# Kernel optimization log

Measured on AMD Instinct MI355X. Metric: run time of the kernel, lower is better.

## Reference

```python
import jax, jax.numpy as jnp
import numpy as np

B, L, D = 1, 512, 1024
NH, NKV, NR = 16, 4, 16
HD, RD = 64, 64
NREP = NH // NKV  # 4
ATTN_SCALE = 1.0 / float(np.sqrt(HD))
REL_SCALE = 1.0 / float(np.sqrt(RD))


def setup_inputs() -> dict:
    key = jax.random.key(0)
    ks = jax.random.split(key, 9)
    x = jax.random.normal(ks[0], (B, L, D), jnp.float32)
    symbols = jax.random.normal(ks[1], (B, L, D), jnp.float32)
    # standard llama-style RoPE frequencies: [L, HD//2]
    inv_freq = 1.0 / (10000.0 ** (np.arange(0, HD, 2, dtype=np.float32) / HD))
    f = np.outer(np.arange(L, dtype=np.float32), inv_freq)
    freqs_cos = jnp.asarray(np.cos(f), jnp.float32)
    freqs_sin = jnp.asarray(np.sin(f), jnp.float32)
    s = 0.02
    wq_attn = jax.random.normal(ks[2], (D, NH * HD), jnp.float32) * s
    wk_attn = jax.random.normal(ks[3], (D, NKV * HD), jnp.float32) * s
    wq_rel = jax.random.normal(ks[4], (D, NR * RD), jnp.float32) * s
    wk_rel = jax.random.normal(ks[5], (D, NR * RD), jnp.float32) * s
    wr = jax.random.normal(ks[6], (NR, NH * HD), jnp.float32) * s
    wv = jax.random.normal(ks[7], (D, NKV * HD), jnp.float32) * s
    wo = jax.random.normal(ks[8], (NH * HD, NH * HD), jnp.float32) * s
    return dict(x=x, symbols=symbols, freqs_cos=freqs_cos, freqs_sin=freqs_sin,
                wq_attn=wq_attn, wk_attn=wk_attn, wq_rel=wq_rel, wk_rel=wk_rel,
                wr=wr, wv=wv, wo=wo)


def _rope(t, cos, sin):
    # t: [b, l, h, hd]; cos/sin: [l, hd//2]
    tr = t.reshape(t.shape[:-1] + (HD // 2, 2))
    re, im = tr[..., 0], tr[..., 1]
    c = cos[None, :, None, :]
    s = sin[None, :, None, :]
    out = jnp.stack([re * c - im * s, re * s + im * c], axis=-1)
    return out.reshape(t.shape)


def reference(x, symbols, freqs_cos, freqs_sin, wq_attn, wk_attn, wq_rel, wk_rel, wr, wv, wo):
    b, l, _ = x.shape
    q = (x @ wq_attn).reshape(b, l, NH, HD)
    k = (x @ wk_attn).reshape(b, l, NKV, HD)
    qr = (x @ wq_rel).reshape(b, l, NR, RD)
    kr = (x @ wk_rel).reshape(b, l, NR, RD)
    sv = (symbols @ wv).reshape(b, l, NKV, HD)
    q = _rope(q, freqs_cos, freqs_sin)
    k = _rope(k, freqs_cos, freqs_sin)
    # GQA: repeat kv heads consecutively (matches torch repeat_kv expand+reshape)
    k = jnp.repeat(k, NREP, axis=2)
    sv = jnp.repeat(sv, NREP, axis=2)
    scores = jnp.einsum('bihd,bjhd->bhij', q, k) * ATTN_SCALE
    causal = jnp.tril(jnp.ones((l, l), bool))
    scores = jnp.where(causal[None, None], scores, -jnp.inf)
    attn = jax.nn.softmax(scores, axis=-1)  # [b, nh, l, l]
    # relation scores, identity activation, laid out as [b, i, j, nr]
    relations = jnp.einsum('bird,bjrd->bijr', qr, kr) * REL_SCALE
    proj_rel = (relations @ wr).reshape(b, l, l, NH, HD)  # dominant intermediate
    attended_symbols = jnp.einsum('bhij,bjhd->bihd', attn, sv)
    attended_relations = jnp.einsum('bhij,bijhd->bihd', attn, proj_rel)
    out = (attended_symbols + attended_relations).reshape(b, l, NH * HD) @ wo
    return out, attn, relations
```

## Files before the change

kernel.cpp:

```cpp
#include <hip/hip_runtime.h>
#include <math.h>

#define ATTN_SCALE 0.125f
#define REL_SCALE 0.125f

using ushort = unsigned short;
using bf16x8 = __attribute__((ext_vector_type(8))) __bf16;
using floatx4 = __attribute__((ext_vector_type(4))) float;
using ushort8 = __attribute__((ext_vector_type(8))) ushort;
using ushort4v = __attribute__((ext_vector_type(4))) ushort;

__device__ __forceinline__ ushort f2bf(float x) {
  unsigned int u = __builtin_bit_cast(unsigned int, x);
  u += 0x7fffu + ((u >> 16) & 1u);
  return (ushort)(u >> 16);
}

__global__ __launch_bounds__(256) void prep_kernel(
    const float* __restrict__ x, const float* __restrict__ sym,
    const float* __restrict__ wq, const float* __restrict__ wk,
    const float* __restrict__ wqr, const float* __restrict__ wkr,
    const float* __restrict__ wv, const float* __restrict__ wo,
    ushort* __restrict__ xb, ushort* __restrict__ symb,
    ushort* __restrict__ wqT, ushort* __restrict__ wkT, ushort* __restrict__ wqrT,
    ushort* __restrict__ wkrT, ushort* __restrict__ wvT, ushort* __restrict__ woT) {
  if (blockIdx.z == 6) {
    int b = blockIdx.y * 32 + blockIdx.x;
    if (b >= 512) return;
    int idx = b * 256 + threadIdx.x;
    int i4 = idx << 2;
    float4 v = *(const float4*)(x + i4);
    uint2 o;
    o.x = (unsigned)f2bf(v.x) | ((unsigned)f2bf(v.y) << 16);
    o.y = (unsigned)f2bf(v.z) | ((unsigned)f2bf(v.w) << 16);
    *(uint2*)(xb + i4) = o;
    float4 w = *(const float4*)(sym + i4);
    o.x = (unsigned)f2bf(w.x) | ((unsigned)f2bf(w.y) << 16);
    o.y = (unsigned)f2bf(w.z) | ((unsigned)f2bf(w.w) << 16);
    *(uint2*)(symb + i4) = o;
    return;
  }
  __shared__ ushort t[32][33];
  const float* in;
  ushort* out;
  int N;
  switch (blockIdx.z) {
    case 0: in = wq;  out = wqT;  N = 1024; break;
    case 1: in = wk;  out = wkT;  N = 256;  break;
    case 2: in = wqr; out = wqrT; N = 1024; break;
    case 3: in = wkr; out = wkrT; N = 1024; break;
    case 4: in = wv;  out = wvT;  N = 256;  break;
    default: in = wo; out = woT;  N = 1024; break;
  }
  int n0 = blockIdx.x << 5;
  if (n0 >= N) return;
  int k0 = blockIdx.y << 5;
  int tx = threadIdx.x & 31, ty = threadIdx.x >> 5;
#pragma unroll
  for (int rr = 0; rr < 32; rr += 8)
    t[ty + rr][tx] = f2bf(in[(size_t)(k0 + ty + rr) * N + n0 + tx]);
  __syncthreads();
#pragma unroll
  for (int rr = 0; rr < 32; rr += 8)
    out[(size_t)(n0 + ty + rr) * 1024 + k0 + tx] = t[tx][ty + rr];
}

__global__ __launch_bounds__(256) void proj_mfma(
    const ushort* __restrict__ xb, const ushort* __restrict__ symb,
    const ushort* __restrict__ wqT, const ushort* __restrict__ wkT,
    const ushort* __restrict__ wqrT, const ushort* __restrict__ wkrT,
    const ushort* __restrict__ wvT,
    ushort* __restrict__ qb, ushort* __restrict__ kb, ushort* __restrict__ qrb,
    ushort* __restrict__ krb, ushort* __restrict__ svT,
    const float* __restrict__ fcos, const float* __restrict__ fsin) {
  __shared__ ushort As[64][72];
  __shared__ ushort Bs[32][72];
  const int z = blockIdx.z;
  const ushort* A = xb;
  const ushort* Bt;
  ushort* C;
  int N;
  switch (z) {
    case 0: Bt = wqT;  C = qb;  N = 1024; break;
    case 1: Bt = wkT;  C = kb;  N = 256;  break;
    case 2: Bt = wqrT; C = qrb; N = 1024; break;
    case 3: Bt = wkrT; C = krb; N = 1024; break;
    default: A = symb; Bt = wvT; C = svT; N = 256; break;
  }
  const int bn = blockIdx.x << 5;
  if (bn >= N) return;
  const int bm = blockIdx.y << 6;
  const int tid = threadIdx.x;
  const int sr = tid >> 2, sc = (tid & 3) << 4;
  const int br = tid >> 3, bc = (tid & 7) << 3;
  const int lane = tid & 63;
  const int wy = (tid >> 7) & 1, wx = (tid >> 6) & 1;
  const int lm = lane & 15, lq = lane >> 4;
  const ushort* a_rd = &As[32 * wy + lm][lq * 8];
  const ushort* b_rd = &Bs[16 * wx + lm][lq * 8];
  floatx4 acc[2] = {};
  for (int k0 = 0; k0 < 1024; k0 += 64) {
    const ushort* Ap = A + (size_t)(bm + sr) * 1024 + k0 + sc;
    ushort8 av0 = *(const ushort8*)Ap;
    ushort8 av1 = *(const ushort8*)(Ap + 8);
    ushort8 bv = *(const ushort8*)(Bt + (size_t)(bn + br) * 1024 + k0 + bc);
    __syncthreads();
    *(ushort8*)&As[sr][sc] = av0;
    *(ushort8*)&As[sr][sc + 8] = av1;
    *(ushort8*)&Bs[br][bc] = bv;
    __syncthreads();
#pragma unroll
    for (int kh = 0; kh < 2; ++kh) {
      bf16x8 a0 = *(const bf16x8*)(a_rd + kh * 32);
      bf16x8 a1 = *(const bf16x8*)(a_rd + 16 * 72 + kh * 32);
      bf16x8 b0 = *(const bf16x8*)(b_rd + kh * 32);
      acc[0] = __builtin_amdgcn_mfma_f32_16x16x32_bf16(a0, b0, acc[0], 0, 0, 0);
      acc[1] = __builtin_amdgcn_mfma_f32_16x16x32_bf16(a1, b0, acc[1], 0, 0, 0);
    }
  }
  if (z <= 1) {
#pragma unroll
    for (int sy = 0; sy < 2; ++sy)
#pragma unroll
      for (int e = 0; e < 4; ++e) {
        int row = bm + 32 * wy + 16 * sy + 4 * lq + e;
        int col = bn + 16 * wx + lm;
        float v = acc[sy][e];
        float pv = __shfl_xor(v, 1);
        int d = col & 63, p = d >> 1;
        float c = fcos[(row << 5) + p], s = fsin[(row << 5) + p];
        float o = (d & 1) ? fmaf(pv, s, v * c) : fmaf(v, c, -pv * s);
        C[(size_t)row * N + col] = f2bf(o);
      }
  } else if (z == 4) {
#pragma unroll
    for (int sy = 0; sy < 2; ++sy)
#pragma unroll
      for (int e = 0; e < 4; ++e) {
        int row = bm + 32 * wy + 16 * sy + 4 * lq + e;
        int col = bn + 16 * wx + lm;
        svT[(size_t)col * 512 + row] = f2bf(acc[sy][e]);
      }
  } else {
#pragma unroll
    for (int sy = 0; sy < 2; ++sy)
#pragma unroll
      for (int e = 0; e < 4; ++e) {
        int row = bm + 32 * wy + 16 * sy + 4 * lq + e;
        int col = bn + 16 * wx + lm;
        C[(size_t)row * N + col] = f2bf(acc[sy][e]);
      }
  }
}

__global__ __launch_bounds__(256) void relflash_kernel(
    const ushort* __restrict__ qb, const ushort* __restrict__ kb,
    const ushort* __restrict__ svT, const ushort* __restrict__ qrb,
    const ushort* __restrict__ krb, float* __restrict__ attn,
    ushort* __restrict__ attn_b, float* __restrict__ asym,
    float* __restrict__ rel, ushort* __restrict__ rel_bT) {
  __shared__ float S[16][516];
  __shared__ ushort P[16][520];
  const int bx = blockIdx.x;
  const int tid = threadIdx.x, wave = tid >> 6, lane = tid & 63;
  const int lm = lane & 15, lq = lane >> 4;
  if (bx >= 512) {
    const int b = bx - 512;
    const int bi0 = (b >> 4) << 5, bj0 = (b & 15) << 5;
    const int ib = bi0 + ((wave >> 1) << 4), jb = bj0 + ((wave & 1) << 4);
    const ushort* qrow = qrb + (size_t)(ib + lm) * 1024 + lq * 8;
    const ushort* krow = krb + (size_t)(jb + lm) * 1024 + lq * 8;
#pragma unroll
    for (int rq = 0; rq < 4; ++rq) {
      floatx4 acc[4];
#pragma unroll
      for (int rr = 0; rr < 4; ++rr) {
        int roff = ((rq << 2) + rr) << 6;
        bf16x8 a0 = *(const bf16x8*)(qrow + roff);
        bf16x8 a1 = *(const bf16x8*)(qrow + roff + 32);
        bf16x8 b0 = *(const bf16x8*)(krow + roff);
        bf16x8 b1 = *(const bf16x8*)(krow + roff + 32);
        floatx4 t = {0.f, 0.f, 0.f, 0.f};
        t = __builtin_amdgcn_mfma_f32_16x16x32_bf16(a0, b0, t, 0, 0, 0);
        t = __builtin_amdgcn_mfma_f32_16x16x32_bf16(a1, b1, t, 0, 0, 0);
        acc[rr] = t;
      }
#pragma unroll
      for (int e = 0; e < 4; ++e) {
        int i = ib + 4 * lq + e, j = jb + lm;
        float4 v = make_float4(acc[0][e] * REL_SCALE, acc[1][e] * REL_SCALE,
                               acc[2][e] * REL_SCALE, acc[3][e] * REL_SCALE);
        *(float4*)(rel + ((size_t)i * 512 + j) * 16 + (rq << 2)) = v;
        size_t tb = (size_t)i * 8192 + (size_t)(rq << 2) * 512 + j;
        rel_bT[tb]        = f2bf(v.x);
        rel_bT[tb + 512]  = f2bf(v.y);
        rel_bT[tb + 1024] = f2bf(v.z);
        rel_bT[tb + 1536] = f2bf(v.w);
      }
    }
    return;
  }
  const int h = bx >> 5, it = 31 - (bx & 31);
  const int i0 = it << 4, kv = h >> 2;
  const int ntiles = it + 1;
  const ushort* qrow = qb + (size_t)(i0 + lm) * 1024 + (h << 6) + lq * 8;
  bf16x8 a0 = *(const bf16x8*)(qrow);
  bf16x8 a1 = *(const bf16x8*)(qrow + 32);
  for (int jt = wave; jt < ntiles; jt += 4) {
    int jb = jt << 4;
    const ushort* krow = kb + (size_t)(jb + lm) * 256 + (kv << 6) + lq * 8;
    bf16x8 b0 = *(const bf16x8*)(krow);
    bf16x8 b1 = *(const bf16x8*)(krow + 32);
    floatx4 acc = {0.f, 0.f, 0.f, 0.f};
    acc = __builtin_amdgcn_mfma_f32_16x16x32_bf16(a0, b0, acc, 0, 0, 0);
    acc = __builtin_amdgcn_mfma_f32_16x16x32_bf16(a1, b1, acc, 0, 0, 0);
#pragma unroll
    for (int e = 0; e < 4; ++e) S[4 * lq + e][jb + lm] = acc[e] * ATTN_SCALE;
  }
  __syncthreads();
  const int row = tid >> 4, t16 = tid & 15;
  const int i = i0 + row;
  const int nj = ntiles << 4;
  float m = -INFINITY;
  for (int s = 0; (s << 6) < nj; ++s) {
    int j4 = (t16 << 2) + (s << 6);
    float4 v = *(const float4*)&S[row][j4];
    if (j4 + 0 <= i) m = fmaxf(m, v.x);
    if (j4 + 1 <= i) m = fmaxf(m, v.y);
    if (j4 + 2 <= i) m = fmaxf(m, v.z);
    if (j4 + 3 <= i) m = fmaxf(m, v.w);
  }
#pragma unroll
  for (int o = 8; o; o >>= 1) m = fmaxf(m, __shfl_xor(m, o, 16));
  float sum = 0.f;
  for (int s = 0; (s << 6) < nj; ++s) {
    int j4 = (t16 << 2) + (s << 6);
    float4 v = *(const float4*)&S[row][j4];
    v.x = (j4 + 0 <= i) ? __expf(v.x - m) : 0.f;
    v.y = (j4 + 1 <= i) ? __expf(v.y - m) : 0.f;
    v.z = (j4 + 2 <= i) ? __expf(v.z - m) : 0.f;
    v.w = (j4 + 3 <= i) ? __expf(v.w - m) : 0.f;
    sum += v.x + v.y + v.z + v.w;
    *(float4*)&S[row][j4] = v;
  }
#pragma unroll
  for (int o = 8; o; o >>= 1) sum += __shfl_xor(sum, o, 16);
  const float inv = 1.f / sum;
  float* arow = attn + (size_t)h * 262144 + (size_t)i * 512;
  ushort* abrow = attn_b + (size_t)i * 8192 + (size_t)h * 512;
  for (int s = 0; s < 8; ++s) {
    int j4 = (t16 << 2) + (s << 6);
    float4 o4 = {0.f, 0.f, 0.f, 0.f};
    if (j4 < nj) {
      float4 v = *(const float4*)&S[row][j4];
      o4.x = v.x * inv;
      o4.y = v.y * inv;
      o4.z = v.z * inv;
      o4.w = v.w * inv;
    }
    *(float4*)(arow + j4) = o4;
    ushort4v p4;
    p4.x = f2bf(o4.x); p4.y = f2bf(o4.y); p4.z = f2bf(o4.z); p4.w = f2bf(o4.w);
    *(ushort4v*)&P[row][j4] = p4;
    *(ushort4v*)(abrow + j4) = p4;
  }
  __syncthreads();
  const int dbase = wave << 4;
  floatx4 acc2 = {0.f, 0.f, 0.f, 0.f};
  const ushort* svrow = svT + (size_t)((kv << 6) + dbase + lm) * 512;
  const int kmax = (nj + 31) & ~31;
  for (int kt = 0; kt < kmax; kt += 32) {
    bf16x8 pa = *(const bf16x8*)&P[lm][kt + lq * 8];
    bf16x8 pb = *(const bf16x8*)(svrow + kt + lq * 8);
    acc2 = __builtin_amdgcn_mfma_f32_16x16x32_bf16(pa, pb, acc2, 0, 0, 0);
  }
#pragma unroll
  for (int e = 0; e < 4; ++e)
    asym[(size_t)(i0 + 4 * lq + e) * 1024 + (h << 6) + dbase + lm] = acc2[e];
}

__global__ __launch_bounds__(256) void tker_combine(const ushort* __restrict__ attn_b,
                                                    const ushort* __restrict__ rel_bT,
                                                    const float* __restrict__ asym,
                                                    const float* __restrict__ wr,
                                                    ushort* __restrict__ attb) {
  const int i0 = blockIdx.x << 2;
  const int tid = threadIdx.x, wave = tid >> 6, lane = tid & 63;
  const int lm = lane & 15, lq = lane >> 4;
  const int i = i0 + wave;
  __shared__ float Ts[4][16][17];
  floatx4 acc = {0.f, 0.f, 0.f, 0.f};
  const ushort* arow = attn_b + (size_t)i * 8192 + (size_t)lm * 512;
  const ushort* brow = rel_bT + (size_t)i * 8192 + (size_t)lm * 512;
  const int ktiles = (i >> 5) + 1;
  for (int kt = 0; kt < ktiles; ++kt) {
    int k = (kt << 5) + lq * 8;
    bf16x8 a = *(const bf16x8*)(arow + k);
    bf16x8 b = *(const bf16x8*)(brow + k);
    acc = __builtin_amdgcn_mfma_f32_16x16x32_bf16(a, b, acc, 0, 0, 0);
  }
#pragma unroll
  for (int e = 0; e < 4; ++e) Ts[wave][4 * lq + e][lm] = acc[e];
  __syncthreads();
  const int hc = tid >> 4, d4 = (tid & 15) << 2;
  float4 o[4];
#pragma unroll
  for (int iw = 0; iw < 4; ++iw)
    o[iw] = *(const float4*)(asym + (size_t)(i0 + iw) * 1024 + (hc << 6) + d4);
#pragma unroll
  for (int rr = 0; rr < 16; ++rr) {
    float4 w4 = *(const float4*)(wr + (size_t)rr * 1024 + (hc << 6) + d4);
#pragma unroll
    for (int iw = 0; iw < 4; ++iw) {
      float tv = Ts[iw][hc][rr];
      o[iw].x = fmaf(tv, w4.x, o[iw].x);
      o[iw].y = fmaf(tv, w4.y, o[iw].y);
      o[iw].z = fmaf(tv, w4.z, o[iw].z);
      o[iw].w = fmaf(tv, w4.w, o[iw].w);
    }
  }
#pragma unroll
  for (int iw = 0; iw < 4; ++iw) {
    ushort4v ob;
    ob.x = f2bf(o[iw].x); ob.y = f2bf(o[iw].y);
    ob.z = f2bf(o[iw].z); ob.w = f2bf(o[iw].w);
    *(ushort4v*)(attb + (size_t)(i0 + iw) * 1024 + (hc << 6) + d4) = ob;
  }
}

__global__ __launch_bounds__(256) void out_mfma(const ushort* __restrict__ attb,
                                                const ushort* __restrict__ woT,
                                                float* __restrict__ out) {
  __shared__ ushort As[64][72];
  __shared__ ushort Bs[32][72];
  const int bn = blockIdx.x << 5, bm = blockIdx.y << 6;
  const int tid = threadIdx.x;
  const int sr = tid >> 2, sc = (tid & 3) << 4;
  const int br = tid >> 3, bc = (tid & 7) << 3;
  const int lane = tid & 63;
  const int wy = (tid >> 7) & 1, wx = (tid >> 6) & 1;
  const int lm = lane & 15, lq = lane >> 4;
  const ushort* a_rd = &As[32 * wy + lm][lq * 8];
  const ushort* b_rd = &Bs[16 * wx + lm][lq * 8];
  floatx4 acc[2] = {};
  for (int k0 = 0; k0 < 1024; k0 += 64) {
    const ushort* Ap = attb + (size_t)(bm + sr) * 1024 + k0 + sc;
    ushort8 av0 = *(const ushort8*)Ap;
    ushort8 av1 = *(const ushort8*)(Ap + 8);
    ushort8 bv = *(const ushort8*)(woT + (size_t)(bn + br) * 1024 + k0 + bc);
    __syncthreads();
    *(ushort8*)&As[sr][sc] = av0;
    *(ushort8*)&As[sr][sc + 8] = av1;
    *(ushort8*)&Bs[br][bc] = bv;
    __syncthreads();
#pragma unroll
    for (int kh = 0; kh < 2; ++kh) {
      bf16x8 a0 = *(const bf16x8*)(a_rd + kh * 32);
      bf16x8 a1 = *(const bf16x8*)(a_rd + 16 * 72 + kh * 32);
      bf16x8 b0 = *(const bf16x8*)(b_rd + kh * 32);
      acc[0] = __builtin_amdgcn_mfma_f32_16x16x32_bf16(a0, b0, acc[0], 0, 0, 0);
      acc[1] = __builtin_amdgcn_mfma_f32_16x16x32_bf16(a1, b0, acc[1], 0, 0, 0);
    }
  }
#pragma unroll
  for (int sy = 0; sy < 2; ++sy)
#pragma unroll
    for (int e = 0; e < 4; ++e) {
      int row = bm + 32 * wy + 16 * sy + 4 * lq + e;
      int col = bn + 16 * wx + lm;
      out[(size_t)row * 1024 + col] = acc[sy][e];
    }
}

extern "C" void kernel_launch(void* const* d_in, const int* in_sizes, int n_in,
                              void* d_out, int out_size, void* d_ws, size_t ws_size,
                              hipStream_t stream) {
  const float* x       = (const float*)d_in[0];
  const float* symbols = (const float*)d_in[1];
  const float* fcos    = (const float*)d_in[2];
  const float* fsin    = (const float*)d_in[3];
  const float* wq_attn = (const float*)d_in[4];
  const float* wk_attn = (const float*)d_in[5];
  const float* wq_rel  = (const float*)d_in[6];
  const float* wk_rel  = (const float*)d_in[7];
  const float* wr      = (const float*)d_in[8];
  const float* wv      = (const float*)d_in[9];
  const float* wo      = (const float*)d_in[10];

  float* out  = (float*)d_out;
  float* attn = out + 524288;
  float* rel  = attn + 4194304;

  char* wsb = (char*)d_ws;
  const size_t KB = 1024;
  ushort* xb     = (ushort*)(wsb);
  ushort* symb   = (ushort*)(wsb + 1024 * KB);
  ushort* wqT    = (ushort*)(wsb + 2048 * KB);
  ushort* wkT    = (ushort*)(wsb + 4096 * KB);
  ushort* wqrT   = (ushort*)(wsb + 4608 * KB);
  ushort* wkrT   = (ushort*)(wsb + 6656 * KB);
  ushort* wvT    = (ushort*)(wsb + 8704 * KB);
  ushort* woT    = (ushort*)(wsb + 9216 * KB);
  ushort* qb     = (ushort*)(wsb + 11264 * KB);
  ushort* kb     = (ushort*)(wsb + 12288 * KB);
  ushort* qrb    = (ushort*)(wsb + 12544 * KB);
  ushort* krb    = (ushort*)(wsb + 13568 * KB);
  ushort* svT    = (ushort*)(wsb + 14592 * KB);
  float*  asym   = (float*)(wsb + 14848 * KB);
  ushort* attb   = (ushort*)(wsb + 16896 * KB);
  ushort* rel_bT = (ushort*)(wsb + 17920 * KB);
  ushort* attn_b = (ushort*)(wsb + 26112 * KB);

  prep_kernel<<<dim3(32, 32, 7), 256, 0, stream>>>(x, symbols, wq_attn, wk_attn,
                                                   wq_rel, wk_rel, wv, wo,
                                                   xb, symb, wqT, wkT, wqrT, wkrT, wvT, woT);
  proj_mfma<<<dim3(32, 8, 5), 256, 0, stream>>>(xb, symb, wqT, wkT, wqrT, wkrT, wvT,
                                                qb, kb, qrb, krb, svT, fcos, fsin);
  relflash_kernel<<<dim3(768), 256, 0, stream>>>(qb, kb, svT, qrb, krb, attn, attn_b,
                                                 asym, rel, rel_bT);
  tker_combine<<<dim3(128), 256, 0, stream>>>(attn_b, rel_bT, asym, wr, attb);
  out_mfma<<<dim3(32, 8), 256, 0, stream>>>(attb, woT, out);
}
```

Baseline: 153.1 us.

## Fuse input bf16 conversion into projection GEMM and widen combine/output grids

Drops the separate x/symbols fp32-to-bf16 pass from the prep kernel, so the projection GEMM now reads fp32 inputs and converts them while staging into shared memory. The combine kernel now handles one row per block and splits the k-tiles across its four waves, reducing their partial sums in shared memory. The output GEMM uses 32x32 tiles, doubling the block count. The aim is to remove a pass and an intermediate buffer and to give more parallelism to small, under-occupied kernels, at the cost of reading twice the bytes for the A operand and repeating the conversion in every N-tile block.

```diff
diff --git a/kernel.cpp b/kernel.cpp
--- a/kernel.cpp
+++ b/kernel.cpp
@@ -17,29 +17,11 @@
 }
 
 __global__ __launch_bounds__(256) void prep_kernel(
-    const float* __restrict__ x, const float* __restrict__ sym,
     const float* __restrict__ wq, const float* __restrict__ wk,
     const float* __restrict__ wqr, const float* __restrict__ wkr,
     const float* __restrict__ wv, const float* __restrict__ wo,
-    ushort* __restrict__ xb, ushort* __restrict__ symb,
     ushort* __restrict__ wqT, ushort* __restrict__ wkT, ushort* __restrict__ wqrT,
     ushort* __restrict__ wkrT, ushort* __restrict__ wvT, ushort* __restrict__ woT) {
-  if (blockIdx.z == 6) {
-    int b = blockIdx.y * 32 + blockIdx.x;
-    if (b >= 512) return;
-    int idx = b * 256 + threadIdx.x;
-    int i4 = idx << 2;
-    float4 v = *(const float4*)(x + i4);
-    uint2 o;
-    o.x = (unsigned)f2bf(v.x) | ((unsigned)f2bf(v.y) << 16);
-    o.y = (unsigned)f2bf(v.z) | ((unsigned)f2bf(v.w) << 16);
-    *(uint2*)(xb + i4) = o;
-    float4 w = *(const float4*)(sym + i4);
-    o.x = (unsigned)f2bf(w.x) | ((unsigned)f2bf(w.y) << 16);
-    o.y = (unsigned)f2bf(w.z) | ((unsigned)f2bf(w.w) << 16);
-    *(uint2*)(symb + i4) = o;
-    return;
-  }
   __shared__ ushort t[32][33];
   const float* in;
   ushort* out;
@@ -66,7 +48,7 @@
 }
 
 __global__ __launch_bounds__(256) void proj_mfma(
-    const ushort* __restrict__ xb, const ushort* __restrict__ symb,
+    const float* __restrict__ x, const float* __restrict__ symbols,
     const ushort* __restrict__ wqT, const ushort* __restrict__ wkT,
     const ushort* __restrict__ wqrT, const ushort* __restrict__ wkrT,
     const ushort* __restrict__ wvT,
@@ -76,7 +58,7 @@
   __shared__ ushort As[64][72];
   __shared__ ushort Bs[32][72];
   const int z = blockIdx.z;
-  const ushort* A = xb;
+  const float* A = x;
   const ushort* Bt;
   ushort* C;
   int N;
@@ -85,7 +67,7 @@
     case 1: Bt = wkT;  C = kb;  N = 256;  break;
     case 2: Bt = wqrT; C = qrb; N = 1024; break;
     case 3: Bt = wkrT; C = krb; N = 1024; break;
-    default: A = symb; Bt = wvT; C = svT; N = 256; break;
+    default: A = symbols; Bt = wvT; C = svT; N = 256; break;
   }
   const int bn = blockIdx.x << 5;
   if (bn >= N) return;
@@ -100,9 +82,15 @@
   const ushort* b_rd = &Bs[16 * wx + lm][lq * 8];
   floatx4 acc[2] = {};
   for (int k0 = 0; k0 < 1024; k0 += 64) {
-    const ushort* Ap = A + (size_t)(bm + sr) * 1024 + k0 + sc;
-    ushort8 av0 = *(const ushort8*)Ap;
-    ushort8 av1 = *(const ushort8*)(Ap + 8);
+    const float* Ap = A + (size_t)(bm + sr) * 1024 + k0 + sc;
+    float4 f0 = *(const float4*)(Ap);
+    float4 f1 = *(const float4*)(Ap + 4);
+    float4 f2 = *(const float4*)(Ap + 8);
+    float4 f3 = *(const float4*)(Ap + 12);
+    ushort8 av0 = ushort8{f2bf(f0.x), f2bf(f0.y), f2bf(f0.z), f2bf(f0.w),
+                          f2bf(f1.x), f2bf(f1.y), f2bf(f1.z), f2bf(f1.w)};
+    ushort8 av1 = ushort8{f2bf(f2.x), f2bf(f2.y), f2bf(f2.z), f2bf(f2.w),
+                          f2bf(f3.x), f2bf(f3.y), f2bf(f3.z), f2bf(f3.w)};
     ushort8 bv = *(const ushort8*)(Bt + (size_t)(bn + br) * 1024 + k0 + bc);
     __syncthreads();
     *(ushort8*)&As[sr][sc] = av0;
@@ -284,16 +272,15 @@
                                                     const float* __restrict__ asym,
                                                     const float* __restrict__ wr,
                                                     ushort* __restrict__ attb) {
-  const int i0 = blockIdx.x << 2;
+  const int i = blockIdx.x;
   const int tid = threadIdx.x, wave = tid >> 6, lane = tid & 63;
   const int lm = lane & 15, lq = lane >> 4;
-  const int i = i0 + wave;
   __shared__ float Ts[4][16][17];
   floatx4 acc = {0.f, 0.f, 0.f, 0.f};
   const ushort* arow = attn_b + (size_t)i * 8192 + (size_t)lm * 512;
   const ushort* brow = rel_bT + (size_t)i * 8192 + (size_t)lm * 512;
   const int ktiles = (i >> 5) + 1;
-  for (int kt = 0; kt < ktiles; ++kt) {
+  for (int kt = wave; kt < ktiles; kt += 4) {
     int k = (kt << 5) + lq * 8;
     bf16x8 a = *(const bf16x8*)(arow + k);
     bf16x8 b = *(const bf16x8*)(brow + k);
@@ -303,73 +290,55 @@
   for (int e = 0; e < 4; ++e) Ts[wave][4 * lq + e][lm] = acc[e];
   __syncthreads();
   const int hc = tid >> 4, d4 = (tid & 15) << 2;
-  float4 o[4];
-#pragma unroll
-  for (int iw = 0; iw < 4; ++iw)
-    o[iw] = *(const float4*)(asym + (size_t)(i0 + iw) * 1024 + (hc << 6) + d4);
+  float4 o = *(const float4*)(asym + (size_t)i * 1024 + (hc << 6) + d4);
 #pragma unroll
   for (int rr = 0; rr < 16; ++rr) {
+    float tv = Ts[0][hc][rr] + Ts[1][hc][rr] + Ts[2][hc][rr] + Ts[3][hc][rr];
     float4 w4 = *(const float4*)(wr + (size_t)rr * 1024 + (hc << 6) + d4);
-#pragma unroll
-    for (int iw = 0; iw < 4; ++iw) {
-      float tv = Ts[iw][hc][rr];
-      o[iw].x = fmaf(tv, w4.x, o[iw].x);
-      o[iw].y = fmaf(tv, w4.y, o[iw].y);
-      o[iw].z = fmaf(tv, w4.z, o[iw].z);
-      o[iw].w = fmaf(tv, w4.w, o[iw].w);
-    }
-  }
-#pragma unroll
-  for (int iw = 0; iw < 4; ++iw) {
-    ushort4v ob;
-    ob.x = f2bf(o[iw].x); ob.y = f2bf(o[iw].y);
-    ob.z = f2bf(o[iw].z); ob.w = f2bf(o[iw].w);
-    *(ushort4v*)(attb + (size_t)(i0 + iw) * 1024 + (hc << 6) + d4) = ob;
-  }
+    o.x = fmaf(tv, w4.x, o.x);
+    o.y = fmaf(tv, w4.y, o.y);
+    o.z = fmaf(tv, w4.z, o.z);
+    o.w = fmaf(tv, w4.w, o.w);
+  }
+  ushort4v ob;
+  ob.x = f2bf(o.x); ob.y = f2bf(o.y); ob.z = f2bf(o.z); ob.w = f2bf(o.w);
+  *(ushort4v*)(attb + (size_t)i * 1024 + (hc << 6) + d4) = ob;
 }
 
 __global__ __launch_bounds__(256) void out_mfma(const ushort* __restrict__ attb,
                                                 const ushort* __restrict__ woT,
                                                 float* __restrict__ out) {
-  __shared__ ushort As[64][72];
+  __shared__ ushort As[32][72];
   __shared__ ushort Bs[32][72];
-  const int bn = blockIdx.x << 5, bm = blockIdx.y << 6;
+  const int bn = blockIdx.x << 5, bm = blockIdx.y << 5;
   const int tid = threadIdx.x;
-  const int sr = tid >> 2, sc = (tid & 3) << 4;
-  const int br = tid >> 3, bc = (tid & 7) << 3;
+  const int sr = tid >> 3, sc = (tid & 7) << 3;
   const int lane = tid & 63;
   const int wy = (tid >> 7) & 1, wx = (tid >> 6) & 1;
   const int lm = lane & 15, lq = lane >> 4;
-  const ushort* a_rd = &As[32 * wy + lm][lq * 8];
+  const ushort* a_rd = &As[16 * wy + lm][lq * 8];
   const ushort* b_rd = &Bs[16 * wx + lm][lq * 8];
-  floatx4 acc[2] = {};
+  floatx4 acc = {0.f, 0.f, 0.f, 0.f};
   for (int k0 = 0; k0 < 1024; k0 += 64) {
-    const ushort* Ap = attb + (size_t)(bm + sr) * 1024 + k0 + sc;
-    ushort8 av0 = *(const ushort8*)Ap;
-    ushort8 av1 = *(const ushort8*)(Ap + 8);
-    ushort8 bv = *(const ushort8*)(woT + (size_t)(bn + br) * 1024 + k0 + bc);
+    ushort8 av = *(const ushort8*)(attb + (size_t)(bm + sr) * 1024 + k0 + sc);
+    ushort8 bv = *(const ushort8*)(woT + (size_t)(bn + sr) * 1024 + k0 + sc);
     __syncthreads();
-    *(ushort8*)&As[sr][sc] = av0;
-    *(ushort8*)&As[sr][sc + 8] = av1;
-    *(ushort8*)&Bs[br][bc] = bv;
+    *(ushort8*)&As[sr][sc] = av;
+    *(ushort8*)&Bs[sr][sc] = bv;
     __syncthreads();
 #pragma unroll
     for (int kh = 0; kh < 2; ++kh) {
       bf16x8 a0 = *(const bf16x8*)(a_rd + kh * 32);
-      bf16x8 a1 = *(const bf16x8*)(a_rd + 16 * 72 + kh * 32);
       bf16x8 b0 = *(const bf16x8*)(b_rd + kh * 32);
-      acc[0] = __builtin_amdgcn_mfma_f32_16x16x32_bf16(a0, b0, acc[0], 0, 0, 0);
-      acc[1] = __builtin_amdgcn_mfma_f32_16x16x32_bf16(a1, b0, acc[1], 0, 0, 0);
+      acc = __builtin_amdgcn_mfma_f32_16x16x32_bf16(a0, b0, acc, 0, 0, 0);
     }
   }
 #pragma unroll
-  for (int sy = 0; sy < 2; ++sy)
-#pragma unroll
-    for (int e = 0; e < 4; ++e) {
-      int row = bm + 32 * wy + 16 * sy + 4 * lq + e;
-      int col = bn + 16 * wx + lm;
-      out[(size_t)row * 1024 + col] = acc[sy][e];
-    }
+  for (int e = 0; e < 4; ++e) {
+    int row = bm + 16 * wy + 4 * lq + e;
+    int col = bn + 16 * wx + lm;
+    out[(size_t)row * 1024 + col] = acc[e];
+  }
 }
 
 extern "C" void kernel_launch(void* const* d_in, const int* in_sizes, int n_in,
@@ -393,31 +362,28 @@
 
   char* wsb = (char*)d_ws;
   const size_t KB = 1024;
-  ushort* xb     = (ushort*)(wsb);
-  ushort* symb   = (ushort*)(wsb + 1024 * KB);
-  ushort* wqT    = (ushort*)(wsb + 2048 * KB);
-  ushort* wkT    = (ushort*)(wsb + 4096 * KB);
-  ushort* wqrT   = (ushort*)(wsb + 4608 * KB);
-  ushort* wkrT   = (ushort*)(wsb + 6656 * KB);
-  ushort* wvT    = (ushort*)(wsb + 8704 * KB);
-  ushort* woT    = (ushort*)(wsb + 9216 * KB);
-  ushort* qb     = (ushort*)(wsb + 11264 * KB);
-  ushort* kb     = (ushort*)(wsb + 12288 * KB);
-  ushort* qrb    = (ushort*)(wsb + 12544 * KB);
-  ushort* krb    = (ushort*)(wsb + 13568 * KB);
-  ushort* svT    = (ushort*)(wsb + 14592 * KB);
-  float*  asym   = (float*)(wsb + 14848 * KB);
-  ushort* attb   = (ushort*)(wsb + 16896 * KB);
-  ushort* rel_bT = (ushort*)(wsb + 17920 * KB);
-  ushort* attn_b = (ushort*)(wsb + 26112 * KB);
-
-  prep_kernel<<<dim3(32, 32, 7), 256, 0, stream>>>(x, symbols, wq_attn, wk_attn,
-                                                   wq_rel, wk_rel, wv, wo,
-                                                   xb, symb, wqT, wkT, wqrT, wkrT, wvT, woT);
-  proj_mfma<<<dim3(32, 8, 5), 256, 0, stream>>>(xb, symb, wqT, wkT, wqrT, wkrT, wvT,
+  ushort* wqT    = (ushort*)(wsb);
+  ushort* wkT    = (ushort*)(wsb + 2048 * KB);
+  ushort* wqrT   = (ushort*)(wsb + 2560 * KB);
+  ushort* wkrT   = (ushort*)(wsb + 4608 * KB);
+  ushort* wvT    = (ushort*)(wsb + 6656 * KB);
+  ushort* woT    = (ushort*)(wsb + 7168 * KB);
+  ushort* qb     = (ushort*)(wsb + 9216 * KB);
+  ushort* kb     = (ushort*)(wsb + 10240 * KB);
+  ushort* qrb    = (ushort*)(wsb + 10496 * KB);
+  ushort* krb    = (ushort*)(wsb + 11520 * KB);
+  ushort* svT    = (ushort*)(wsb + 12544 * KB);
+  float*  asym   = (float*)(wsb + 12800 * KB);
+  ushort* attb   = (ushort*)(wsb + 14848 * KB);
+  ushort* rel_bT = (ushort*)(wsb + 15872 * KB);
+  ushort* attn_b = (ushort*)(wsb + 24064 * KB);
+
+  prep_kernel<<<dim3(32, 32, 6), 256, 0, stream>>>(wq_attn, wk_attn, wq_rel, wk_rel,
+                                                   wv, wo, wqT, wkT, wqrT, wkrT, wvT, woT);
+  proj_mfma<<<dim3(32, 8, 5), 256, 0, stream>>>(x, symbols, wqT, wkT, wqrT, wkrT, wvT,
                                                 qb, kb, qrb, krb, svT, fcos, fsin);
   relflash_kernel<<<dim3(768), 256, 0, stream>>>(qb, kb, svT, qrb, krb, attn, attn_b,
                                                  asym, rel, rel_bT);
-  tker_combine<<<dim3(128), 256, 0, stream>>>(attn_b, rel_bT, asym, wr, attb);
-  out_mfma<<<dim3(32, 8), 256, 0, stream>>>(attb, woT, out);
-}
+  tker_combine<<<dim3(512), 256, 0, stream>>>(attn_b, rel_bT, asym, wr, attb);
+  out_mfma<<<dim3(32, 16), 256, 0, stream>>>(attb, woT, out);
+}
```

Result: slower. 156.4 us (+2.1%).

## Replace LDS-staged projection and output GEMMs with per-wave direct-load MFMA tiles

Applied to the files above, without the earlier changes.

The projection and output GEMMs no longer stage A/B tiles through shared memory with two barriers per k-step. Instead each wave loads its MFMA fragments straight from global memory, computing a 32x32 tile in the projection kernel and a 16x16 tile in the output kernel, with a flat 1D grid. This removes LDS traffic and block-wide synchronisation, relying on L2/cache reuse across waves, but each wave now issues more redundant global loads. The output kernel also loses register reuse because each fragment feeds only one MFMA.

```diff
diff --git a/kernel.cpp b/kernel.cpp
--- a/kernel.cpp
+++ b/kernel.cpp
@@ -65,7 +65,7 @@
     out[(size_t)(n0 + ty + rr) * 1024 + k0 + tx] = t[tx][ty + rr];
 }
 
-__global__ __launch_bounds__(256) void proj_mfma(
+__global__ __launch_bounds__(256) void proj_direct(
     const ushort* __restrict__ xb, const ushort* __restrict__ symb,
     const ushort* __restrict__ wqT, const ushort* __restrict__ wkT,
     const ushort* __restrict__ wqrT, const ushort* __restrict__ wkrT,
@@ -73,83 +73,75 @@
     ushort* __restrict__ qb, ushort* __restrict__ kb, ushort* __restrict__ qrb,
     ushort* __restrict__ krb, ushort* __restrict__ svT,
     const float* __restrict__ fcos, const float* __restrict__ fsin) {
-  __shared__ ushort As[64][72];
-  __shared__ ushort Bs[32][72];
-  const int z = blockIdx.z;
+  const int tid = threadIdx.x, wave = tid >> 6, lane = tid & 63;
+  const int lm = lane & 15, lq = lane >> 4;
+  const int t = blockIdx.x * 4 + wave;
   const ushort* A = xb;
   const ushort* Bt;
   ushort* C;
-  int N;
-  switch (z) {
-    case 0: Bt = wqT;  C = qb;  N = 1024; break;
-    case 1: Bt = wkT;  C = kb;  N = 256;  break;
-    case 2: Bt = wqrT; C = qrb; N = 1024; break;
-    case 3: Bt = wkrT; C = krb; N = 1024; break;
-    default: A = symb; Bt = wvT; C = svT; N = 256; break;
-  }
-  const int bn = blockIdx.x << 5;
-  if (bn >= N) return;
-  const int bm = blockIdx.y << 6;
-  const int tid = threadIdx.x;
-  const int sr = tid >> 2, sc = (tid & 3) << 4;
-  const int br = tid >> 3, bc = (tid & 7) << 3;
-  const int lane = tid & 63;
-  const int wy = (tid >> 7) & 1, wx = (tid >> 6) & 1;
-  const int lm = lane & 15, lq = lane >> 4;
-  const ushort* a_rd = &As[32 * wy + lm][lq * 8];
-  const ushort* b_rd = &Bs[16 * wx + lm][lq * 8];
-  floatx4 acc[2] = {};
-  for (int k0 = 0; k0 < 1024; k0 += 64) {
-    const ushort* Ap = A + (size_t)(bm + sr) * 1024 + k0 + sc;
-    ushort8 av0 = *(const ushort8*)Ap;
-    ushort8 av1 = *(const ushort8*)(Ap + 8);
-    ushort8 bv = *(const ushort8*)(Bt + (size_t)(bn + br) * 1024 + k0 + bc);
-    __syncthreads();
-    *(ushort8*)&As[sr][sc] = av0;
-    *(ushort8*)&As[sr][sc + 8] = av1;
-    *(ushort8*)&Bs[br][bc] = bv;
-    __syncthreads();
-#pragma unroll
-    for (int kh = 0; kh < 2; ++kh) {
-      bf16x8 a0 = *(const bf16x8*)(a_rd + kh * 32);
-      bf16x8 a1 = *(const bf16x8*)(a_rd + 16 * 72 + kh * 32);
-      bf16x8 b0 = *(const bf16x8*)(b_rd + kh * 32);
-      acc[0] = __builtin_amdgcn_mfma_f32_16x16x32_bf16(a0, b0, acc[0], 0, 0, 0);
-      acc[1] = __builtin_amdgcn_mfma_f32_16x16x32_bf16(a1, b0, acc[1], 0, 0, 0);
-    }
-  }
-  if (z <= 1) {
+  int N, lo, ecase;
+  if (t < 512)       { Bt = wqT;  C = qb;  N = 1024; lo = t;        ecase = 0; }
+  else if (t < 640)  { Bt = wkT;  C = kb;  N = 256;  lo = t - 512;  ecase = 0; }
+  else if (t < 1152) { Bt = wqrT; C = qrb; N = 1024; lo = t - 640;  ecase = 1; }
+  else if (t < 1664) { Bt = wkrT; C = krb; N = 1024; lo = t - 1152; ecase = 1; }
+  else               { A = symb; Bt = wvT; C = svT; N = 256; lo = t - 1664; ecase = 2; }
+  int wm, wn;
+  if (N == 1024) { wm = (lo >> 5) << 5; wn = (lo & 31) << 5; }
+  else           { wm = (lo >> 3) << 5; wn = (lo & 7) << 5; }
+
+  const ushort* arow0 = A + (size_t)(wm + lm) * 1024 + lq * 8;
+  const ushort* arow1 = arow0 + 16 * 1024;
+  const ushort* brow0 = Bt + (size_t)(wn + lm) * 1024 + lq * 8;
+  const ushort* brow1 = brow0 + 16 * 1024;
+  floatx4 acc[2][2] = {};
+  for (int k = 0; k < 1024; k += 32) {
+    bf16x8 a0 = *(const bf16x8*)(arow0 + k);
+    bf16x8 a1 = *(const bf16x8*)(arow1 + k);
+    bf16x8 b0 = *(const bf16x8*)(brow0 + k);
+    bf16x8 b1 = *(const bf16x8*)(brow1 + k);
+    acc[0][0] = __builtin_amdgcn_mfma_f32_16x16x32_bf16(a0, b0, acc[0][0], 0, 0, 0);
+    acc[0][1] = __builtin_amdgcn_mfma_f32_16x16x32_bf16(a0, b1, acc[0][1], 0, 0, 0);
+    acc[1][0] = __builtin_amdgcn_mfma_f32_16x16x32_bf16(a1, b0, acc[1][0], 0, 0, 0);
+    acc[1][1] = __builtin_amdgcn_mfma_f32_16x16x32_bf16(a1, b1, acc[1][1], 0, 0, 0);
+  }
+  if (ecase == 0) {
 #pragma unroll
     for (int sy = 0; sy < 2; ++sy)
 #pragma unroll
-      for (int e = 0; e < 4; ++e) {
-        int row = bm + 32 * wy + 16 * sy + 4 * lq + e;
-        int col = bn + 16 * wx + lm;
-        float v = acc[sy][e];
-        float pv = __shfl_xor(v, 1);
-        int d = col & 63, p = d >> 1;
-        float c = fcos[(row << 5) + p], s = fsin[(row << 5) + p];
-        float o = (d & 1) ? fmaf(pv, s, v * c) : fmaf(v, c, -pv * s);
-        C[(size_t)row * N + col] = f2bf(o);
-      }
-  } else if (z == 4) {
+      for (int sx = 0; sx < 2; ++sx)
+#pragma unroll
+        for (int e = 0; e < 4; ++e) {
+          int row = wm + 16 * sy + 4 * lq + e;
+          int col = wn + 16 * sx + lm;
+          float v = acc[sy][sx][e];
+          float pv = __shfl_xor(v, 1);
+          int d = col & 63, pp = d >> 1;
+          float c = fcos[(row << 5) + pp], s = fsin[(row << 5) + pp];
+          float o = (d & 1) ? fmaf(pv, s, v * c) : fmaf(v, c, -pv * s);
+          C[(size_t)row * N + col] = f2bf(o);
+        }
+  } else if (ecase == 2) {
 #pragma unroll
     for (int sy = 0; sy < 2; ++sy)
 #pragma unroll
-      for (int e = 0; e < 4; ++e) {
-        int row = bm + 32 * wy + 16 * sy + 4 * lq + e;
-        int col = bn + 16 * wx + lm;
-        svT[(size_t)col * 512 + row] = f2bf(acc[sy][e]);
-      }
+      for (int sx = 0; sx < 2; ++sx)
+#pragma unroll
+        for (int e = 0; e < 4; ++e) {
+          int row = wm + 16 * sy + 4 * lq + e;
+          int col = wn + 16 * sx + lm;
+          svT[(size_t)col * 512 + row] = f2bf(acc[sy][sx][e]);
+        }
   } else {
 #pragma unroll
     for (int sy = 0; sy < 2; ++sy)
 #pragma unroll
-      for (int e = 0; e < 4; ++e) {
-        int row = bm + 32 * wy + 16 * sy + 4 * lq + e;
-        int col = bn + 16 * wx + lm;
-        C[(size_t)row * N + col] = f2bf(acc[sy][e]);
-      }
+      for (int sx = 0; sx < 2; ++sx)
+#pragma unroll
+        for (int e = 0; e < 4; ++e) {
+          int row = wm + 16 * sy + 4 * lq + e;
+          int col = wn + 16 * sx + lm;
+          C[(size_t)row * N + col] = f2bf(acc[sy][sx][e]);
+        }
   }
 }
 
@@ -328,48 +320,24 @@
   }
 }
 
-__global__ __launch_bounds__(256) void out_mfma(const ushort* __restrict__ attb,
-                                                const ushort* __restrict__ woT,
-                                                float* __restrict__ out) {
-  __shared__ ushort As[64][72];
-  __shared__ ushort Bs[32][72];
-  const int bn = blockIdx.x << 5, bm = blockIdx.y << 6;
-  const int tid = threadIdx.x;
-  const int sr = tid >> 2, sc = (tid & 3) << 4;
-  const int br = tid >> 3, bc = (tid & 7) << 3;
-  const int lane = tid & 63;
-  const int wy = (tid >> 7) & 1, wx = (tid >> 6) & 1;
+__global__ __launch_bounds__(256) void out_direct(const ushort* __restrict__ attb,
+                                                  const ushort* __restrict__ woT,
+                                                  float* __restrict__ out) {
+  const int tid = threadIdx.x, wave = tid >> 6, lane = tid & 63;
   const int lm = lane & 15, lq = lane >> 4;
-  const ushort* a_rd = &As[32 * wy + lm][lq * 8];
-  const ushort* b_rd = &Bs[16 * wx + lm][lq * 8];
-  floatx4 acc[2] = {};
-  for (int k0 = 0; k0 < 1024; k0 += 64) {
-    const ushort* Ap = attb + (size_t)(bm + sr) * 1024 + k0 + sc;
-    ushort8 av0 = *(const ushort8*)Ap;
-    ushort8 av1 = *(const ushort8*)(Ap + 8);
-    ushort8 bv = *(const ushort8*)(woT + (size_t)(bn + br) * 1024 + k0 + bc);
-    __syncthreads();
-    *(ushort8*)&As[sr][sc] = av0;
-    *(ushort8*)&As[sr][sc + 8] = av1;
-    *(ushort8*)&Bs[br][bc] = bv;
-    __syncthreads();
-#pragma unroll
-    for (int kh = 0; kh < 2; ++kh) {
-      bf16x8 a0 = *(const bf16x8*)(a_rd + kh * 32);
-      bf16x8 a1 = *(const bf16x8*)(a_rd + 16 * 72 + kh * 32);
-      bf16x8 b0 = *(const bf16x8*)(b_rd + kh * 32);
-      acc[0] = __builtin_amdgcn_mfma_f32_16x16x32_bf16(a0, b0, acc[0], 0, 0, 0);
-      acc[1] = __builtin_amdgcn_mfma_f32_16x16x32_bf16(a1, b0, acc[1], 0, 0, 0);
-    }
-  }
-#pragma unroll
-  for (int sy = 0; sy < 2; ++sy)
-#pragma unroll
-    for (int e = 0; e < 4; ++e) {
-      int row = bm + 32 * wy + 16 * sy + 4 * lq + e;
-      int col = bn + 16 * wx + lm;
-      out[(size_t)row * 1024 + col] = acc[sy][e];
-    }
+  const int t = blockIdx.x * 4 + wave;
+  const int wm = (t >> 6) << 4, wn = (t & 63) << 4;
+  const ushort* arow = attb + (size_t)(wm + lm) * 1024 + lq * 8;
+  const ushort* brow = woT + (size_t)(wn + lm) * 1024 + lq * 8;
+  floatx4 acc = {0.f, 0.f, 0.f, 0.f};
+  for (int k = 0; k < 1024; k += 32) {
+    bf16x8 a = *(const bf16x8*)(arow + k);
+    bf16x8 b = *(const bf16x8*)(brow + k);
+    acc = __builtin_amdgcn_mfma_f32_16x16x32_bf16(a, b, acc, 0, 0, 0);
+  }
+#pragma unroll
+  for (int e = 0; e < 4; ++e)
+    out[(size_t)(wm + 4 * lq + e) * 1024 + wn + lm] = acc[e];
 }
 
 extern "C" void kernel_launch(void* const* d_in, const int* in_sizes, int n_in,
@@ -414,10 +382,10 @@
   prep_kernel<<<dim3(32, 32, 7), 256, 0, stream>>>(x, symbols, wq_attn, wk_attn,
                                                    wq_rel, wk_rel, wv, wo,
                                                    xb, symb, wqT, wkT, wqrT, wkrT, wvT, woT);
-  proj_mfma<<<dim3(32, 8, 5), 256, 0, stream>>>(xb, symb, wqT, wkT, wqrT, wkrT, wvT,
-                                                qb, kb, qrb, krb, svT, fcos, fsin);
+  proj_direct<<<dim3(448), 256, 0, stream>>>(xb, symb, wqT, wkT, wqrT, wkrT, wvT,
+                                             qb, kb, qrb, krb, svT, fcos, fsin);
   relflash_kernel<<<dim3(768), 256, 0, stream>>>(qb, kb, svT, qrb, krb, attn, attn_b,
                                                  asym, rel, rel_bT);
   tker_combine<<<dim3(128), 256, 0, stream>>>(attn_b, rel_bT, asym, wr, attb);
-  out_mfma<<<dim3(32, 8), 256, 0, stream>>>(attb, woT, out);
-}
+  out_direct<<<dim3(512), 256, 0, stream>>>(attb, woT, out);
+}
```

Measured after the change: 173.1 us. +13.0%, slower.
